# Kernel tuning notes

Measured on AMD Instinct MI355X. Metric: run time of the kernel, lower is better.

The kernel has to match this reference:

```python
import jax, jax.numpy as jnp
import numpy as np
import math

B, S, D = 4, 4096, 1024
H = 16
HD = D // H          # head_dim = 64
M = 256              # nb_features (random projection dim)


def _orthogonal_gaussian(key, m, d):
    # FAVOR+ orthogonal random features: blocks of d orthogonal rows,
    # each row rescaled to a chi-distributed norm (norm of a d-dim gaussian).
    n_blocks = int(math.ceil(m / d))
    keys = jax.random.split(key, n_blocks + 1)
    blocks = []
    for i in range(n_blocks):
        g = jax.random.normal(keys[i], (d, d), dtype=jnp.float32)
        q, _ = jnp.linalg.qr(g)
        blocks.append(q.T)
    W = jnp.concatenate(blocks, axis=0)[:m]  # [m, d]
    norms = jnp.linalg.norm(
        jax.random.normal(keys[-1], (m, d), dtype=jnp.float32), axis=1, keepdims=True)
    return W * norms


def _softmax_kernel(x, proj, is_query, eps=1e-4):
    # x: [b,h,s,d]; proj: [m,d]. Standard FAVOR+ positive softmax features.
    d = x.shape[-1]
    ratio = proj.shape[0] ** -0.5
    x = x * (d ** -0.25)
    u = jnp.einsum('bhsd,md->bhsm', x, proj)  # projection
    diag = 0.5 * jnp.sum(x * x, axis=-1, keepdims=True)  # [b,h,s,1]
    if is_query:
        stab = jnp.max(u, axis=-1, keepdims=True)
    else:
        stab = jnp.max(u, axis=(-1, -2), keepdims=True)
    return ratio * (jnp.exp(u - diag - stab) + eps)


def performer_attention(Q, K, V, mask, proj):
    # Q,K,V: [b,h,s,d], mask: [b,s]
    scale = HD ** -0.25
    m4 = mask[:, None, :, None]
    Qs = Q * scale
    Ks = K * scale * m4
    Vs = V * m4
    q_prime = _softmax_kernel(Qs, proj, is_query=True)   # [b,h,s,m]
    k_prime = _softmax_kernel(Ks, proj, is_query=False)  # [b,h,s,m]
    # linear attention: O(s*m*d)
    kv = jnp.einsum('bhsm,bhsd->bhmd', k_prime, Vs)      # [b,h,m,d]
    z = 1.0 / (jnp.einsum('bhsm,bhm->bhs', q_prime, jnp.sum(k_prime, axis=2)) + 1e-6)
    out = jnp.einsum('bhsm,bhmd->bhsd', q_prime, kv) * z[..., None]
    return out


def setup_inputs() -> dict:
    key = jax.random.key(0)
    ks = jax.random.split(key, 9)
    X = jax.random.normal(ks[0], (B, S, D), dtype=jnp.float32)
    mask = jnp.ones((B, S), dtype=jnp.float32)
    s = D ** -0.5
    Wq = jax.random.normal(ks[1], (D, D), dtype=jnp.float32) * s
    bq = jnp.zeros((D,), dtype=jnp.float32)
    Wk = jax.random.normal(ks[2], (D, D), dtype=jnp.float32) * s
    bk = jnp.zeros((D,), dtype=jnp.float32)
    Wv = jax.random.normal(ks[3], (D, D), dtype=jnp.float32) * s
    bv = jnp.zeros((D,), dtype=jnp.float32)
    proj = _orthogonal_gaussian(ks[4], M, HD)
    return {"X": X, "mask": mask, "Wq": Wq, "bq": bq, "Wk": Wk, "bk": bk,
            "Wv": Wv, "bv": bv, "proj": proj}


def _split_heads(x):
    b, s, _ = x.shape
    return x.reshape(b, s, H, HD).transpose(0, 2, 1, 3)


def reference(X, mask, Wq, bq, Wk, bk, Wv, bv, proj):
    Q = _split_heads(X @ Wq + bq)
    K = _split_heads(X @ Wk + bk)
    V = _split_heads(X @ Wv + bv)
    attn = performer_attention(Q, K, V, mask, proj)  # [b,h,s,hd]
    out = attn.transpose(0, 2, 1, 3).reshape(B, S, D)
    return out
```

## Files before the change

kernel.cpp:

```cpp
#include <hip/hip_runtime.h>
#include <stdint.h>

#define DEVI static __device__ __forceinline__

typedef unsigned short u16;
typedef unsigned int u32;
typedef __attribute__((ext_vector_type(8))) short short8;
typedef __attribute__((ext_vector_type(4))) float f32x4;
typedef __attribute__((ext_vector_type(4))) unsigned short ushort4_t;

#define BB 4
#define SS 4096
#define DD 1024
#define HH 16
#define HDD 64
#define MM 256
#define BHN 64

DEVI u16 f2bf(float f) {
    u32 u = __float_as_uint(f);
    u += 0x7fffu + ((u >> 16) & 1u);
    return (u16)(u >> 16);
}
DEVI float bf2f(u16 h) { return __uint_as_float(((u32)h) << 16); }

typedef __attribute__((address_space(1))) const unsigned int as1_u32;
typedef __attribute__((address_space(3))) unsigned int as3_u32;
DEVI void load_lds16(const void* g, void* lds) {
    __builtin_amdgcn_global_load_lds((as1_u32*)g, (as3_u32*)lds, 16, 0, 0);
}


__global__ void conv_bf16(const float* __restrict__ src, u16* __restrict__ dst, int n4) {
    int i = blockIdx.x * 256 + threadIdx.x;
    if (i < n4) {
        float4 v = reinterpret_cast<const float4*>(src)[i];
        ushort4_t o = { f2bf(v.x), f2bf(v.y), f2bf(v.z), f2bf(v.w) };
        reinterpret_cast<ushort4_t*>(dst)[i] = o;
    }
}

__global__ void conv_w(const float* __restrict__ Wq, const float* __restrict__ Wk,
                       const float* __restrict__ Wv, u16* __restrict__ Wt) {
    __shared__ float tile[64][65];
    const int jt = blockIdx.x, kt = blockIdx.y;
    const float* src = (jt < 16) ? Wq : (jt < 32) ? Wk : Wv;
    const int j0 = (jt & 15) * 64, k0 = kt * 64;
    const int t = threadIdx.x;
    for (int i = 0; i < 16; ++i) {
        int lin = t + i * 256;
        int kl = lin >> 6, jl = lin & 63;
        tile[kl][jl] = src[(size_t)(k0 + kl) * DD + j0 + jl];
    }
    __syncthreads();
    const int jg0 = jt * 64;
    for (int i = 0; i < 16; ++i) {
        int lin = t + i * 256;
        int jl = lin >> 6, kl = lin & 63;
        Wt[(size_t)(jg0 + jl) * DD + k0 + kl] = f2bf(tile[kl][jl]);
    }
}

__global__ __launch_bounds__(512, 2) void gemm1_big(
    const u16* __restrict__ Xbf, const u16* __restrict__ Wt,
    const float* __restrict__ bq, const float* __restrict__ bk, const float* __restrict__ bv,
    const float* __restrict__ mask,
    u16* __restrict__ Qh, u16* __restrict__ Kh, u16* __restrict__ Vt,
    float* __restrict__ dq, float* __restrict__ dk)
{
    extern __shared__ __align__(16) char smem[];
    const int tid = threadIdx.x, l = tid & 63, wv = tid >> 6;
    const int wm = wv >> 2, wn = wv & 3;
    const int bid = blockIdx.x;
    const int xcd = bid & 7, i6 = bid >> 3;
    const int bx = xcd * 8 + i6 / 12, by = i6 % 12;
    const int row0 = bx * 256, col0 = by * 256;

    const int srow = tid >> 3;
    const int scol = ((tid & 7) ^ (srow & 7)) * 8;

    #define ABUF(p) ((char*)smem + (p) * 32768)
    #define BBUF(p) ((char*)smem + 65536 + (p) * 32768)
    #define STA(p, kt, r) load_lds16(Xbf + (size_t)(row0 + (r)*64 + srow) * DD + (kt)*64 + scol, \
                                     ABUF(p) + (r)*8192 + wv*1024)
    #define STB(p, kt, r) load_lds16(Wt + (size_t)(col0 + (r)*64 + srow) * DD + (kt)*64 + scol, \
                                     BBUF(p) + (r)*8192 + wv*1024)

    STA(0,0,0); STA(0,0,1); STA(0,0,2); STA(0,0,3);
    STB(0,0,0); STB(0,0,1); STB(0,0,2); STB(0,0,3);
    asm volatile("s_waitcnt vmcnt(0)" ::: "memory");
    __builtin_amdgcn_s_barrier();
    __builtin_amdgcn_sched_barrier(0);

    f32x4 acc[8][4] = {};
    const int arow_b = wm * 128 + (l & 15);
    const int brow_b = wn * 64 + (l & 15);
    const int cb_b = (l >> 4) * 16;
    const int lx = (l & 7) << 4;

    for (int kt = 0; kt < 16; ++kt) {
        const int p = kt & 1, pn = p ^ 1;
        const bool more = (kt + 1) < 16;
        short8 bfr[4][2];
#pragma unroll
        for (int q = 0; q < 4; ++q) {
            if (more) {
                if (q == 0)      { STA(pn, kt + 1, 0); STA(pn, kt + 1, 1); }
                else if (q == 1) { STA(pn, kt + 1, 2); STA(pn, kt + 1, 3); }
                else if (q == 2) { STB(pn, kt + 1, 0); STB(pn, kt + 1, 1); }
                else             { STB(pn, kt + 1, 2); STB(pn, kt + 1, 3); }
            }
            if (q == 0) {
#pragma unroll
                for (int nf = 0; nf < 4; ++nf) {
                    const int br = brow_b + nf * 16;
#pragma unroll
                    for (int ks = 0; ks < 2; ++ks)
                        bfr[nf][ks] = *(const short8*)(BBUF(p) + br * 128 + ((cb_b + ks * 64) ^ lx));
                }
            }
            short8 a[2][2];
#pragma unroll
            for (int i = 0; i < 2; ++i) {
                const int ar = arow_b + (q * 2 + i) * 16;
#pragma unroll
                for (int ks = 0; ks < 2; ++ks)
                    a[i][ks] = *(const short8*)(ABUF(p) + ar * 128 + ((cb_b + ks * 64) ^ lx));
            }
            __builtin_amdgcn_s_setprio(1);
#pragma unroll
            for (int i = 0; i < 2; ++i)
#pragma unroll
                for (int nf = 0; nf < 4; ++nf) {
                    acc[q*2+i][nf] = __builtin_amdgcn_mfma_f32_16x16x32_bf16(a[i][0], bfr[nf][0], acc[q*2+i][nf], 0, 0, 0);
                    acc[q*2+i][nf] = __builtin_amdgcn_mfma_f32_16x16x32_bf16(a[i][1], bfr[nf][1], acc[q*2+i][nf], 0, 0, 0);
                }
            __builtin_amdgcn_s_setprio(0);
            __builtin_amdgcn_sched_barrier(0);
        }
        asm volatile("s_waitcnt vmcnt(0)" ::: "memory");
        __builtin_amdgcn_s_barrier();
        __builtin_amdgcn_sched_barrier(0);
    }

    const int region = by >> 2;
    const int h = ((by & 3) << 2) + wn;
    const int rg = row0 + wm * 128;
    const int b = rg >> 12;
    const int sb = rg & 4095;
    const size_t bh = (size_t)(b * HH + h);
    const int dd = l & 15;
    const int jbase = ((by & 3) << 8) + wn * 64;

    if (region == 0) {
        float bias[4];
#pragma unroll
        for (int nf = 0; nf < 4; ++nf) bias[nf] = bq[jbase + nf * 16 + dd];
#pragma unroll
        for (int mf = 0; mf < 8; ++mf) {
            float ds4[4];
#pragma unroll
            for (int g = 0; g < 4; ++g) {
                const int s = sb + mf * 16 + ((l >> 4) << 2) + g;
                float dsum = 0.f;
#pragma unroll
                for (int nf = 0; nf < 4; ++nf) {
                    u16 hv = f2bf((acc[mf][nf][g] + bias[nf]) * 0.125f);
                    Qh[(bh * SS + s) * HDD + nf * 16 + dd] = hv;
                    float fv = bf2f(hv);
                    dsum += fv * fv;
                }
                dsum += __shfl_xor(dsum, 1);
                dsum += __shfl_xor(dsum, 2);
                dsum += __shfl_xor(dsum, 4);
                dsum += __shfl_xor(dsum, 8);
                ds4[g] = 0.5f * dsum;
            }
            if (dd == 0)
                *(float4*)(dq + bh * SS + sb + mf * 16 + ((l >> 4) << 2)) =
                    make_float4(ds4[0], ds4[1], ds4[2], ds4[3]);
        }
    } else if (region == 1) {
        float bias[4];
#pragma unroll
        for (int nf = 0; nf < 4; ++nf) bias[nf] = bk[jbase + nf * 16 + dd];
#pragma unroll
        for (int mf = 0; mf < 8; ++mf) {
            float ds4[4];
#pragma unroll
            for (int g = 0; g < 4; ++g) {
                const int s = sb + mf * 16 + ((l >> 4) << 2) + g;
                const float m = mask[b * SS + s];
                float dsum = 0.f;
#pragma unroll
                for (int nf = 0; nf < 4; ++nf) {
                    u16 hv = f2bf((acc[mf][nf][g] + bias[nf]) * m * 0.125f);
                    Kh[(bh * SS + s) * HDD + nf * 16 + dd] = hv;
                    float fv = bf2f(hv);
                    dsum += fv * fv;
                }
                dsum += __shfl_xor(dsum, 1);
                dsum += __shfl_xor(dsum, 2);
                dsum += __shfl_xor(dsum, 4);
                dsum += __shfl_xor(dsum, 8);
                ds4[g] = 0.5f * dsum;
            }
            if (dd == 0)
                *(float4*)(dk + bh * SS + sb + mf * 16 + ((l >> 4) << 2)) =
                    make_float4(ds4[0], ds4[1], ds4[2], ds4[3]);
        }
    } else {
        float bias[4];
#pragma unroll
        for (int nf = 0; nf < 4; ++nf) bias[nf] = bv[jbase + nf * 16 + dd];
#pragma unroll
        for (int mf = 0; mf < 8; ++mf) {
            const int s0 = sb + mf * 16 + ((l >> 4) << 2);
#pragma unroll
            for (int nf = 0; nf < 4; ++nf) {
                ushort4_t pk;
#pragma unroll
                for (int g = 0; g < 4; ++g) {
                    const float m = mask[b * SS + s0 + g];
                    pk[g] = f2bf((acc[mf][nf][g] + bias[nf]) * m);
                }
                *(ushort4_t*)(Vt + (bh * HDD + nf * 16 + dd) * SS + s0) = pk;
            }
        }
    }
    #undef ABUF
    #undef BBUF
    #undef STA
    #undef STB
}

__global__ __launch_bounds__(256, 2) void kv_fused(
    const u16* __restrict__ Kh, const u16* __restrict__ Vt,
    const u16* __restrict__ projb, const float* __restrict__ dk,
    float* __restrict__ kv_part, float* __restrict__ ksum_part,
    float* __restrict__ vsum_part, float* __restrict__ lstab)
{
    extern __shared__ __align__(16) char ksm[];
    #define KLDS(b) ((char*)ksm + (b) * 8192)
    #define VLDS(b) ((char*)ksm + 24576 + (b) * 8192)
    u16* Kp = (u16*)((char*)ksm + 49152);
    const int tid = threadIdx.x, l = tid & 63, wv = tid >> 6;
    const int ck = blockIdx.x, bh = blockIdx.y;
    short8 pb[4][2];
#pragma unroll
    for (int nf = 0; nf < 4; ++nf)
#pragma unroll
        for (int ks = 0; ks < 2; ++ks)
            pb[nf][ks] = *(const short8*)(projb + (wv * 64 + nf * 16 + (l & 15)) * HDD + ks * 32 + (l >> 4) * 8);
    const size_t sbase = (size_t)bh * SS + ck * 512;

    #define KSTAGE(buf, it8) do { \
        const int s0_ = (it8) * 64; \
        _Pragma("unroll") \
        for (int c = 0; c < 2; ++c) { \
            const int rb = wv * 16 + c * 8; \
            const int r = rb + (l >> 3); \
            const int sc = ((l & 7) ^ (r & 7)) * 8; \
            load_lds16(Kh + (sbase + s0_ + r) * HDD + sc, KLDS(buf) + rb * 128); \
        } \
    } while (0)
    #define VSTAGE(buf, it8) do { \
        const int s0_ = (it8) * 64; \
        _Pragma("unroll") \
        for (int c = 0; c < 2; ++c) { \
            const int rb = wv * 16 + c * 8; \
            const int r = rb + (l >> 3); \
            const int sc = ((l & 7) ^ (r & 7)) * 8; \
            load_lds16(Vt + ((size_t)bh * HDD + r) * SS + ck * 512 + s0_ + sc, VLDS(buf) + rb * 128); \
        } \
    } while (0)

    float wmax = -3.0e38f;
    KSTAGE(0, 0);
    for (int it = 0; it < 8; ++it) {
        if (it + 1 < 8) {
            KSTAGE((it + 1) % 3, it + 1);
            asm volatile("s_waitcnt vmcnt(2)" ::: "memory");
        } else {
            asm volatile("s_waitcnt vmcnt(0)" ::: "memory");
        }
        __syncthreads();
        const int bs = it % 3;
#pragma unroll
        for (int sf = 0; sf < 4; ++sf) {
            const int s = sf * 16 + (l & 15);
            f32x4 u4[4] = {};
#pragma unroll
            for (int ks = 0; ks < 2; ++ks) {
                short8 ak = *(const short8*)(KLDS(bs) + s * 128 + ((ks * 64 + (l >> 4) * 16) ^ ((s & 7) << 4)));
#pragma unroll
                for (int nf = 0; nf < 4; ++nf)
                    u4[nf] = __builtin_amdgcn_mfma_f32_16x16x32_bf16(ak, pb[nf][ks], u4[nf], 0, 0, 0);
            }
#pragma unroll
            for (int nf = 0; nf < 4; ++nf)
#pragma unroll
                for (int g = 0; g < 4; ++g) wmax = fmaxf(wmax, u4[nf][g]);
        }
    }
#pragma unroll
    for (int o = 1; o < 64; o <<= 1) wmax = fmaxf(wmax, __shfl_xor(wmax, o));
    if (l == 0) lstab[((size_t)ck * BHN + bh) * 4 + wv] = wmax;
    const float stab = wmax;

    f32x4 acc[4][4] = {};
    float ksc[4] = {0.f, 0.f, 0.f, 0.f};
    float vsc[4] = {0.f, 0.f, 0.f, 0.f};
    KSTAGE(0, 0); VSTAGE(0, 0);
    for (int it = 0; it < 8; ++it) {
        if (it + 1 < 8) {
            KSTAGE((it + 1) % 3, it + 1);
            VSTAGE((it + 1) % 3, it + 1);
            asm volatile("s_waitcnt vmcnt(4)" ::: "memory");
        } else {
            asm volatile("s_waitcnt vmcnt(0)" ::: "memory");
        }
        __syncthreads();
        const int bs = it % 3;
        const int s0 = it * 64;
#pragma unroll
        for (int sf = 0; sf < 4; ++sf) {
            const int s = sf * 16 + (l & 15);
            f32x4 u4[4] = {};
#pragma unroll
            for (int ks = 0; ks < 2; ++ks) {
                short8 ak = *(const short8*)(KLDS(bs) + s * 128 + ((ks * 64 + (l >> 4) * 16) ^ ((s & 7) << 4)));
#pragma unroll
                for (int nf = 0; nf < 4; ++nf)
                    u4[nf] = __builtin_amdgcn_mfma_f32_16x16x32_bf16(ak, pb[nf][ks], u4[nf], 0, 0, 0);
            }
            const int srow = sf * 16 + (l >> 4) * 4;
            const float4 dkv = *(const float4*)(dk + sbase + s0 + srow);
#pragma unroll
            for (int nf = 0; nf < 4; ++nf) {
                const int m = wv * 64 + nf * 16 + (l & 15);
                u16 h0 = f2bf(__expf(u4[nf][0] - dkv.x - stab));
                u16 h1 = f2bf(__expf(u4[nf][1] - dkv.y - stab));
                u16 h2 = f2bf(__expf(u4[nf][2] - dkv.z - stab));
                u16 h3 = f2bf(__expf(u4[nf][3] - dkv.w - stab));
                ksc[nf] += bf2f(h0) + bf2f(h1) + bf2f(h2) + bf2f(h3);
                uint2 w; w.x = (u32)h0 | ((u32)h1 << 16); w.y = (u32)h2 | ((u32)h3 << 16);
                *(uint2*)((char*)Kp + m * 128 + ((srow * 2) ^ ((m & 7) << 4))) = w;
            }
        }
        __syncthreads();
#pragma unroll
        for (int ks = 0; ks < 2; ++ks) {
            short8 am[4], bv8[4];
#pragma unroll
            for (int mf = 0; mf < 4; ++mf) {
                const int m = wv * 64 + mf * 16 + (l & 15);
                am[mf] = *(const short8*)((const char*)Kp + m * 128 + ((ks * 64 + (l >> 4) * 16) ^ ((m & 7) << 4)));
            }
#pragma unroll
            for (int nf = 0; nf < 4; ++nf) {
                const int d = nf * 16 + (l & 15);
                bv8[nf] = *(const short8*)(VLDS(bs) + d * 128 + ((ks * 64 + (l >> 4) * 16) ^ ((d & 7) << 4)));
                float vs = 0.f;
#pragma unroll
                for (int e = 0; e < 8; ++e) vs += bf2f((u16)bv8[nf][e]);
                vsc[nf] += vs;
            }
#pragma unroll
            for (int mf = 0; mf < 4; ++mf)
#pragma unroll
                for (int nf = 0; nf < 4; ++nf)
                    acc[mf][nf] = __builtin_amdgcn_mfma_f32_16x16x32_bf16(am[mf], bv8[nf], acc[mf][nf], 0, 0, 0);
        }
    }
    const size_t pbase = (size_t)ck * BHN + bh;
#pragma unroll
    for (int nf = 0; nf < 4; ++nf) {
        float v = ksc[nf];
        v += __shfl_xor(v, 16);
        v += __shfl_xor(v, 32);
        if (l < 16) ksum_part[pbase * MM + wv * 64 + nf * 16 + l] = v;
        float w = vsc[nf];
        w += __shfl_xor(w, 16);
        w += __shfl_xor(w, 32);
        if (wv == 0 && l < 16) vsum_part[pbase * HDD + nf * 16 + l] = w;
    }
#pragma unroll
    for (int mf = 0; mf < 4; ++mf)
#pragma unroll
        for (int nf = 0; nf < 4; ++nf)
            *(f32x4*)(kv_part + (pbase * HDD + nf * 16 + (l & 15)) * MM + wv * 64 + mf * 16 + (l >> 4) * 4) = acc[mf][nf];
    #undef KLDS
    #undef VLDS
    #undef KSTAGE
    #undef VSTAGE
}

__global__ void reduceB3(const float* __restrict__ kv_part, const float* __restrict__ ksum_part,
                         const float* __restrict__ vsum_part, const float* __restrict__ lstab,
                         u16* __restrict__ Bmat) {
    __shared__ float f[8][4];
    const int bh = blockIdx.x, n = blockIdx.y, t = threadIdx.x;
    if (t < 32) {
        float lv = lstab[((size_t)(t >> 2) * BHN + bh) * 4 + (t & 3)];
        float g = lv;
#pragma unroll
        for (int o = 1; o < 32; o <<= 1) g = fmaxf(g, __shfl_xor(g, o));
        f[t >> 2][t & 3] = __expf(lv - g);
    }
    __syncthreads();
    const int grp = t >> 6;
    float s = 0.f;
    if (n < 64) {
        float vsg = 0.f;
#pragma unroll
        for (int ck = 0; ck < 8; ++ck) {
            vsg += vsum_part[((size_t)ck * BHN + bh) * HDD + n];
            s += kv_part[(((size_t)ck * BHN + bh) * HDD + n) * MM + t] * f[ck][grp];
        }
        s = 0.0625f * (s + 1e-4f * vsg);
    } else if (n == 64) {
#pragma unroll
        for (int ck = 0; ck < 8; ++ck)
            s += ksum_part[((size_t)ck * BHN + bh) * MM + t] * f[ck][grp];
        s = 0.0625f * (s + 1e-4f * 4096.0f);
    }
    Bmat[((size_t)bh * 80 + n) * MM + t] = (n <= 64) ? f2bf(s) : (u16)0;
}

__global__ __launch_bounds__(256) void out_fused(
    const u16* __restrict__ Qh, const u16* __restrict__ projb,
    const float* __restrict__ dq, const u16* __restrict__ Bmat,
    float* __restrict__ out)
{
    __shared__ __align__(16) u16 Qlds[64 * 64];
    __shared__ __align__(16) u16 qlds[64 * 256];
    __shared__ float red[4][64];
    const int tid = threadIdx.x, l = tid & 63, wv = tid >> 6;
    const int rt = blockIdx.x, bh = blockIdx.y;
    const size_t srowbase = (size_t)bh * SS + rt * 64;
#pragma unroll
    for (int c = 0; c < 2; ++c) {
        const int rb = wv * 16 + c * 8;
        const int r = rb + (l >> 3);
        load_lds16(Qh + (srowbase + r) * HDD + (((l & 7) ^ (r & 7)) * 8), (char*)Qlds + rb * 128);
    }
    short8 pa[4][2];
#pragma unroll
    for (int mf = 0; mf < 4; ++mf)
#pragma unroll
        for (int ks = 0; ks < 2; ++ks)
            pa[mf][ks] = *(const short8*)(projb + (wv * 64 + mf * 16 + (l & 15)) * HDD + ks * 32 + (l >> 4) * 8);
    __syncthreads();
    f32x4 u[4][4] = {};
#pragma unroll
    for (int ks = 0; ks < 2; ++ks) {
        short8 bq8[4];
#pragma unroll
        for (int nf = 0; nf < 4; ++nf) {
            const int s = nf * 16 + (l & 15);
            bq8[nf] = *(const short8*)((const char*)Qlds + s * 128 + ((ks * 64 + (l >> 4) * 16) ^ ((s & 7) << 4)));
        }
#pragma unroll
        for (int mf = 0; mf < 4; ++mf)
#pragma unroll
            for (int nf = 0; nf < 4; ++nf)
                u[mf][nf] = __builtin_amdgcn_mfma_f32_16x16x32_bf16(pa[mf][ks], bq8[nf], u[mf][nf], 0, 0, 0);
    }
#pragma unroll
    for (int nf = 0; nf < 4; ++nf) {
        float v = -3.0e38f;
#pragma unroll
        for (int mf = 0; mf < 4; ++mf)
#pragma unroll
            for (int g = 0; g < 4; ++g) v = fmaxf(v, u[mf][nf][g]);
        v = fmaxf(v, __shfl_xor(v, 16));
        v = fmaxf(v, __shfl_xor(v, 32));
        if ((l >> 4) == 0) red[wv][nf * 16 + l] = v;
    }
    __syncthreads();
#pragma unroll
    for (int nf = 0; nf < 4; ++nf) {
        const int s = nf * 16 + (l & 15);
        const float mx = fmaxf(fmaxf(red[0][s], red[1][s]), fmaxf(red[2][s], red[3][s]));
        const float dg = dq[srowbase + s];
#pragma unroll
        for (int mf = 0; mf < 4; ++mf) {
            u16 h0 = f2bf(0.0625f * (__expf(u[mf][nf][0] - dg - mx) + 1e-4f));
            u16 h1 = f2bf(0.0625f * (__expf(u[mf][nf][1] - dg - mx) + 1e-4f));
            u16 h2 = f2bf(0.0625f * (__expf(u[mf][nf][2] - dg - mx) + 1e-4f));
            u16 h3 = f2bf(0.0625f * (__expf(u[mf][nf][3] - dg - mx) + 1e-4f));
            uint2 w; w.x = (u32)h0 | ((u32)h1 << 16); w.y = (u32)h2 | ((u32)h3 << 16);
            const int mb = (wv * 64 + mf * 16 + (l >> 4) * 4) * 2;
            *(uint2*)((char*)qlds + s * 512 + (mb ^ ((s & 7) << 4))) = w;
        }
    }
    __syncthreads();
    const u16* bbase = Bmat + (size_t)bh * 20480;
    f32x4 acc[4][2] = {};
#pragma unroll
    for (int kt = 0; kt < 8; ++kt) {
        short8 aq[4], bb[2];
#pragma unroll
        for (int mf = 0; mf < 4; ++mf) {
            const int s = mf * 16 + (l & 15);
            aq[mf] = *(const short8*)((const char*)qlds + s * 512 + ((kt * 64 + (l >> 4) * 16) ^ ((s & 7) << 4)));
        }
        bb[0] = *(const short8*)(bbase + (wv * 16 + (l & 15)) * 256 + kt * 32 + (l >> 4) * 8);
        bb[1] = *(const short8*)(bbase + (64 + (l & 15)) * 256 + kt * 32 + (l >> 4) * 8);
#pragma unroll
        for (int mf = 0; mf < 4; ++mf)
#pragma unroll
            for (int nf = 0; nf < 2; ++nf)
                acc[mf][nf] = __builtin_amdgcn_mfma_f32_16x16x32_bf16(aq[mf], bb[nf], acc[mf][nf], 0, 0, 0);
    }
    const int b = bh >> 4, h = bh & 15;
#pragma unroll
    for (int mf = 0; mf < 4; ++mf) {
#pragma unroll
        for (int g = 0; g < 4; ++g) {
            const float den = __shfl(acc[mf][1][g], (l & 48));
            const float z = 1.0f / (den + 1e-6f);
            const int s = rt * 64 + mf * 16 + (l >> 4) * 4 + g;
            out[((size_t)b * SS + s) * DD + h * HDD + wv * 16 + (l & 15)] = acc[mf][0][g] * z;
        }
    }
}

extern "C" void kernel_launch(void* const* d_in, const int* in_sizes, int n_in,
                              void* d_out, int out_size, void* d_ws, size_t ws_size,
                              hipStream_t stream)
{
    const float* X    = (const float*)d_in[0];
    const float* mask = (const float*)d_in[1];
    const float* Wq   = (const float*)d_in[2];
    const float* bq   = (const float*)d_in[3];
    const float* Wk   = (const float*)d_in[4];
    const float* bk   = (const float*)d_in[5];
    const float* Wv   = (const float*)d_in[6];
    const float* bv   = (const float*)d_in[7];
    const float* proj = (const float*)d_in[8];
    float* out = (float*)d_out;

    char* p = (char*)d_ws;
    u16* Xbf = (u16*)p;
    float* kv_part = (float*)p; p += 33554432;
    u16* Wt = (u16*)p;    p += 6291456;
    u16* projb = (u16*)p; p += 32768;
    u16* Qh = (u16*)p;    p += 33554432;
    u16* Kh = (u16*)p;    p += 33554432;
    u16* Vt = (u16*)p;    p += 33554432;
    float* dq = (float*)p; p += 1048576;
    float* dk = (float*)p; p += 1048576;
    float* ksum_part = (float*)p; p += 524288;
    u16* Bmat = (u16*)p;  p += 2621440;
    float* vsum_part = (float*)p; p += 131072;
    float* lstab = (float*)p; p += 8192;
    if (ws_size < 145924096ull) return;

    hipFuncSetAttribute((const void*)gemm1_big, hipFuncAttributeMaxDynamicSharedMemorySize, 131072);
    hipFuncSetAttribute((const void*)kv_fused, hipFuncAttributeMaxDynamicSharedMemorySize, 81920);

    conv_bf16<<<16384, 256, 0, stream>>>(X, Xbf, 4194304);
    conv_w<<<dim3(48, 16), 256, 0, stream>>>(Wq, Wk, Wv, Wt);
    conv_bf16<<<16, 256, 0, stream>>>(proj, projb, 4096);
    gemm1_big<<<768, 512, 131072, stream>>>(Xbf, Wt, bq, bk, bv, mask, Qh, Kh, Vt, dq, dk);
    kv_fused<<<dim3(8, 64), 256, 81920, stream>>>(Kh, Vt, projb, dk, kv_part, ksum_part, vsum_part, lstab);
    reduceB3<<<dim3(64, 80), 256, 0, stream>>>(kv_part, ksum_part, vsum_part, lstab, Bmat);
    out_fused<<<dim3(64, 64), 256, 0, stream>>>(Qh, projb, dq, Bmat, out);
}
```

Before: 260.1 us.

## Replace two-pass key max with online running-max rescaling in KV accumulation

Removes the separate first pass over K that computed the per-wave maximum of the projected keys. The maximum is now tracked on the fly per 64-row tile, and the kv accumulators and key sums are rescaled whenever it grows, as in online softmax. This drops one full K reload and one projection MFMA pass per chunk. In exchange it adds a per-tile wave reduction, a possible rescale of 64 accumulator values, and more live registers from holding all 16 u4 fragments at once, which may raise register pressure.

```diff
diff --git a/kernel.cpp b/kernel.cpp
--- a/kernel.cpp
+++ b/kernel.cpp
@@ -275,39 +275,7 @@
         } \
     } while (0)
 
-    float wmax = -3.0e38f;
-    KSTAGE(0, 0);
-    for (int it = 0; it < 8; ++it) {
-        if (it + 1 < 8) {
-            KSTAGE((it + 1) % 3, it + 1);
-            asm volatile("s_waitcnt vmcnt(2)" ::: "memory");
-        } else {
-            asm volatile("s_waitcnt vmcnt(0)" ::: "memory");
-        }
-        __syncthreads();
-        const int bs = it % 3;
-#pragma unroll
-        for (int sf = 0; sf < 4; ++sf) {
-            const int s = sf * 16 + (l & 15);
-            f32x4 u4[4] = {};
-#pragma unroll
-            for (int ks = 0; ks < 2; ++ks) {
-                short8 ak = *(const short8*)(KLDS(bs) + s * 128 + ((ks * 64 + (l >> 4) * 16) ^ ((s & 7) << 4)));
-#pragma unroll
-                for (int nf = 0; nf < 4; ++nf)
-                    u4[nf] = __builtin_amdgcn_mfma_f32_16x16x32_bf16(ak, pb[nf][ks], u4[nf], 0, 0, 0);
-            }
-#pragma unroll
-            for (int nf = 0; nf < 4; ++nf)
-#pragma unroll
-                for (int g = 0; g < 4; ++g) wmax = fmaxf(wmax, u4[nf][g]);
-        }
-    }
-#pragma unroll
-    for (int o = 1; o < 64; o <<= 1) wmax = fmaxf(wmax, __shfl_xor(wmax, o));
-    if (l == 0) lstab[((size_t)ck * BHN + bh) * 4 + wv] = wmax;
-    const float stab = wmax;
-
+    float mrun = -3.0e38f;
     f32x4 acc[4][4] = {};
     float ksc[4] = {0.f, 0.f, 0.f, 0.f};
     float vsc[4] = {0.f, 0.f, 0.f, 0.f};
@@ -323,26 +291,52 @@
         __syncthreads();
         const int bs = it % 3;
         const int s0 = it * 64;
+        f32x4 u4[4][4];
 #pragma unroll
         for (int sf = 0; sf < 4; ++sf) {
+#pragma unroll
+            for (int nf = 0; nf < 4; ++nf) u4[sf][nf] = (f32x4){0.f, 0.f, 0.f, 0.f};
             const int s = sf * 16 + (l & 15);
-            f32x4 u4[4] = {};
 #pragma unroll
             for (int ks = 0; ks < 2; ++ks) {
                 short8 ak = *(const short8*)(KLDS(bs) + s * 128 + ((ks * 64 + (l >> 4) * 16) ^ ((s & 7) << 4)));
 #pragma unroll
                 for (int nf = 0; nf < 4; ++nf)
-                    u4[nf] = __builtin_amdgcn_mfma_f32_16x16x32_bf16(ak, pb[nf][ks], u4[nf], 0, 0, 0);
-            }
+                    u4[sf][nf] = __builtin_amdgcn_mfma_f32_16x16x32_bf16(ak, pb[nf][ks], u4[sf][nf], 0, 0, 0);
+            }
+        }
+        float pmax = -3.0e38f;
+#pragma unroll
+        for (int sf = 0; sf < 4; ++sf)
+#pragma unroll
+            for (int nf = 0; nf < 4; ++nf)
+#pragma unroll
+                for (int g = 0; g < 4; ++g) pmax = fmaxf(pmax, u4[sf][nf][g]);
+#pragma unroll
+        for (int o = 1; o < 64; o <<= 1) pmax = fmaxf(pmax, __shfl_xor(pmax, o));
+        if (pmax > mrun) {
+            const float fac = __expf(mrun - pmax);
+            mrun = pmax;
+#pragma unroll
+            for (int mf = 0; mf < 4; ++mf)
+#pragma unroll
+                for (int nf = 0; nf < 4; ++nf)
+#pragma unroll
+                    for (int g = 0; g < 4; ++g) acc[mf][nf][g] *= fac;
+#pragma unroll
+            for (int nf = 0; nf < 4; ++nf) ksc[nf] *= fac;
+        }
+#pragma unroll
+        for (int sf = 0; sf < 4; ++sf) {
             const int srow = sf * 16 + (l >> 4) * 4;
             const float4 dkv = *(const float4*)(dk + sbase + s0 + srow);
 #pragma unroll
             for (int nf = 0; nf < 4; ++nf) {
                 const int m = wv * 64 + nf * 16 + (l & 15);
-                u16 h0 = f2bf(__expf(u4[nf][0] - dkv.x - stab));
-                u16 h1 = f2bf(__expf(u4[nf][1] - dkv.y - stab));
-                u16 h2 = f2bf(__expf(u4[nf][2] - dkv.z - stab));
-                u16 h3 = f2bf(__expf(u4[nf][3] - dkv.w - stab));
+                u16 h0 = f2bf(__expf(u4[sf][nf][0] - dkv.x - mrun));
+                u16 h1 = f2bf(__expf(u4[sf][nf][1] - dkv.y - mrun));
+                u16 h2 = f2bf(__expf(u4[sf][nf][2] - dkv.z - mrun));
+                u16 h3 = f2bf(__expf(u4[sf][nf][3] - dkv.w - mrun));
                 ksc[nf] += bf2f(h0) + bf2f(h1) + bf2f(h2) + bf2f(h3);
                 uint2 w; w.x = (u32)h0 | ((u32)h1 << 16); w.y = (u32)h2 | ((u32)h3 << 16);
                 *(uint2*)((char*)Kp + m * 128 + ((srow * 2) ^ ((m & 7) << 4))) = w;
@@ -373,6 +367,7 @@
                     acc[mf][nf] = __builtin_amdgcn_mfma_f32_16x16x32_bf16(am[mf], bv8[nf], acc[mf][nf], 0, 0, 0);
         }
     }
+    if (l == 0) lstab[((size_t)ck * BHN + bh) * 4 + wv] = mrun;
     const size_t pbase = (size_t)ck * BHN + bh;
 #pragma unroll
     for (int nf = 0; nf < 4; ++nf) {
```

Result: no change. 255.5 us (-1.8%).
